# Optimization experiments

Hardware: AMD Instinct MI355X
Metric: run time of the kernel (lower is better)

Reference implementation:

```python
import jax, jax.numpy as jnp
import numpy as np

N = 100_000          # nodes
E = 1_600_000        # edges (avg degree 16)
IN_C, OUT_C = 256, 128


def setup_inputs() -> dict:
    key = jax.random.key(0)
    k1, k2, k3, k4, k5 = jax.random.split(key, 5)
    X = jax.random.normal(k1, (N, IN_C), dtype=jnp.float32)
    # nn.Linear(in, out, bias=False) weight has shape [out, in]
    W = jax.random.normal(k2, (OUT_C, IN_C), dtype=jnp.float32) * (1.0 / np.sqrt(IN_C))
    A_rows = jnp.sort(jax.random.randint(k3, (E,), 0, N, dtype=jnp.int32))
    A_cols = jax.random.randint(k4, (E,), 0, N, dtype=jnp.int32)
    # positive values mimicking symmetric-normalized adjacency entries
    A_vals = jax.random.uniform(k5, (E,), dtype=jnp.float32) * (1.0 / 16.0)
    return {"X": X, "W": W, "A_rows": A_rows, "A_cols": A_cols, "A_vals": A_vals}


def reference(X, W, A_rows, A_cols, A_vals):
    # X = self._linear(X)  ->  X @ W^T   [N, OUT_C]
    H = jnp.einsum("ni,oi->no", X, W)
    # X = torch.sparse.mm(A_hat, X): out[r] += v * H[c] for each edge (r, c, v)
    msgs = A_vals[:, None] * H[A_cols]                      # [E, OUT_C]
    out = jax.ops.segment_sum(msgs, A_rows, num_segments=N)  # [N, OUT_C]
    return out
```

## Files before the change

kernel.cpp:

```cpp
#include <hip/hip_runtime.h>
#include <hip/hip_bf16.h>

#define NNODES 100000
#define NEDGES 1600000
#define IN_C   256
#define OUT_C  128

typedef short bf16x8 __attribute__((ext_vector_type(8)));
typedef float f32x4  __attribute__((ext_vector_type(4)));

static __device__ __forceinline__ unsigned short f2bf(float f) {
    union { float f; unsigned u; } c; c.f = f;
    unsigned r = c.u + 0x7fffu + ((c.u >> 16) & 1u);
    return (unsigned short)(r >> 16);
}

union BF8 { bf16x8 v; unsigned short s[8]; };

__global__ __launch_bounds__(512, 4) void gemm_xwt(const float* __restrict__ X,
                                                   const float* __restrict__ W,
                                                   unsigned char* __restrict__ H8,
                                                   float* __restrict__ scale) {
    __shared__ unsigned short Wsh[128 * 256];

    const int tid  = threadIdx.x;
    const int lane = tid & 63;
    const int wid  = tid >> 6;

#pragma unroll
    for (int p = 0; p < 16; ++p) {
        int idx = p * 512 + tid;
        int n   = idx >> 6;
        int c4  = idx & 63;
        float4 v = *(const float4*)(W + (size_t)n * IN_C + c4 * 4);
        int byte = (n * 512 + c4 * 8) ^ ((n & 7) << 4);
        *(ushort4*)((char*)Wsh + byte) =
            make_ushort4(f2bf(v.x), f2bf(v.y), f2bf(v.z), f2bf(v.w));
    }
    __syncthreads();

    const int r0   = blockIdx.x * 128 + wid * 16;
    int arow = r0 + (lane & 15);
    if (arow > NNODES - 1) arow = NNODES - 1;
    const float* xrow = X + (size_t)arow * IN_C + (lane >> 4) * 8;

    f32x4 acc[8] = {};
#pragma unroll
    for (int ks = 0; ks < 8; ++ks) {
        float4 a0 = *(const float4*)(xrow + ks * 32);
        float4 a1 = *(const float4*)(xrow + ks * 32 + 4);
        BF8 t;
        t.s[0] = f2bf(a0.x); t.s[1] = f2bf(a0.y); t.s[2] = f2bf(a0.z); t.s[3] = f2bf(a0.w);
        t.s[4] = f2bf(a1.x); t.s[5] = f2bf(a1.y); t.s[6] = f2bf(a1.z); t.s[7] = f2bf(a1.w);
        const int kb = ks * 64 + (lane >> 4) * 16;
#pragma unroll
        for (int n8 = 0; n8 < 8; ++n8) {
            int nr   = n8 * 16 + (lane & 15);
            int byte = (nr * 512 + kb) ^ ((nr & 7) << 4);
            bf16x8 b = *(const bf16x8*)((const char*)Wsh + byte);
            acc[n8] = __builtin_amdgcn_mfma_f32_16x16x32_bf16(t.v, b, acc[n8],
                                                              0, 0, 0);
        }
    }

    float amax[4];
#pragma unroll
    for (int r = 0; r < 4; ++r) {
        float m = 0.f;
#pragma unroll
        for (int n8 = 0; n8 < 8; ++n8) m = fmaxf(m, fabsf(acc[n8][r]));
        amax[r] = m;
    }
#pragma unroll
    for (int d = 1; d < 16; d <<= 1)
#pragma unroll
        for (int r = 0; r < 4; ++r)
            amax[r] = fmaxf(amax[r], __shfl_xor(amax[r], d));

#pragma unroll
    for (int r = 0; r < 4; ++r) {
        int grow = r0 + (lane >> 4) * 4 + r;
        if (grow < NNODES) {
            float am  = amax[r];
            float inv = am > 0.f ? 127.f / am : 0.f;
            if ((lane & 15) == 0) scale[grow] = am * (1.f / 127.f);
#pragma unroll
            for (int n8 = 0; n8 < 8; ++n8) {
                float q = rintf(acc[n8][r] * inv);
                q = fminf(127.f, fmaxf(-127.f, q));
                H8[(size_t)grow * OUT_C + n8 * 16 + (lane & 15)] =
                    (unsigned char)((int)q + 128);
            }
        }
    }
}

__global__ __launch_bounds__(256) void build_rowptr(const int* __restrict__ rows,
                                                    int* __restrict__ rowptr) {
    int r = blockIdx.x * 256 + threadIdx.x;
    if (r > NNODES) return;
    int lo = 0, hi = NEDGES;
    while (lo < hi) {
        int mid = (lo + hi) >> 1;
        if (rows[mid] < r) lo = mid + 1; else hi = mid;
    }
    rowptr[r] = lo;
}

static __device__ __forceinline__ void fma8(float acc[8], float* sw,
                                            uint2 u, float v) {
    *sw += v;
    acc[0] += v * (float)( u.x        & 0xffu);
    acc[1] += v * (float)((u.x >>  8) & 0xffu);
    acc[2] += v * (float)((u.x >> 16) & 0xffu);
    acc[3] += v * (float)( u.x >> 24);
    acc[4] += v * (float)( u.y        & 0xffu);
    acc[5] += v * (float)((u.y >>  8) & 0xffu);
    acc[6] += v * (float)((u.y >> 16) & 0xffu);
    acc[7] += v * (float)( u.y >> 24);
}

__global__ __launch_bounds__(256) void spmm_rows(const uint2* __restrict__ H2,
                                                 const int* __restrict__ rowptr,
                                                 const int* __restrict__ cols,
                                                 const float* __restrict__ vals,
                                                 const float* __restrict__ scale,
                                                 float* __restrict__ out) {
    const int wid  = threadIdx.x >> 6;
    const int lane = threadIdx.x & 63;
    const int g    = lane >> 4;
    const int cg   = lane & 15;

    const int rowA = (blockIdx.x * 4 + wid) * 2;
    const int sA = rowptr[rowA];
    const int eA = rowptr[rowA + 1];
    const int eB = rowptr[rowA + 2];

    float accA[8], accB[8];
#pragma unroll
    for (int t = 0; t < 8; ++t) { accA[t] = 0.f; accB[t] = 0.f; }
    float swA = 0.f, swB = 0.f;

    int baseA = sA, baseB = eA;
    while (baseA < eA || baseB < eB) {
        int cntA = eA - baseA; cntA = cntA < 0 ? 0 : (cntA > 64 ? 64 : cntA);
        int cntB = eB - baseB; cntB = cntB < 0 ? 0 : (cntB > 64 ? 64 : cntB);

        int   ecA = 0, ecB = 0;
        float evA = 0.f, evB = 0.f;
        if (lane < cntA) { ecA = cols[baseA + lane]; evA = vals[baseA + lane] * scale[ecA]; }
        if (lane < cntB) { ecB = cols[baseB + lane]; evB = vals[baseB + lane] * scale[ecB]; }

        const int mx = cntA > cntB ? cntA : cntB;
        for (int j = 0; j < mx; j += 16) {
            const bool dA0 = j      < cntA, dA1 = j +  4 < cntA,
                       dA2 = j + 8  < cntA, dA3 = j + 12 < cntA;
            const bool dB0 = j      < cntB, dB1 = j +  4 < cntB,
                       dB2 = j + 8  < cntB, dB3 = j + 12 < cntB;

            int cA0 = __shfl(ecA, j + g),      cB0 = __shfl(ecB, j + g);
            int cA1 = __shfl(ecA, j + 4 + g),  cB1 = __shfl(ecB, j + 4 + g);
            int cA2 = __shfl(ecA, j + 8 + g),  cB2 = __shfl(ecB, j + 8 + g);
            int cA3 = __shfl(ecA, j + 12 + g), cB3 = __shfl(ecB, j + 12 + g);
            uint2 uA0, uA1, uA2, uA3, uB0, uB1, uB2, uB3;
            if (dA0) uA0 = H2[(size_t)cA0 * 16 + cg];
            if (dB0) uB0 = H2[(size_t)cB0 * 16 + cg];
            if (dA1) uA1 = H2[(size_t)cA1 * 16 + cg];
            if (dB1) uB1 = H2[(size_t)cB1 * 16 + cg];
            if (dA2) uA2 = H2[(size_t)cA2 * 16 + cg];
            if (dB2) uB2 = H2[(size_t)cB2 * 16 + cg];
            if (dA3) uA3 = H2[(size_t)cA3 * 16 + cg];
            if (dB3) uB3 = H2[(size_t)cB3 * 16 + cg];

            if (dA0) fma8(accA, &swA, uA0, __shfl(evA, j + g));
            if (dB0) fma8(accB, &swB, uB0, __shfl(evB, j + g));
            if (dA1) fma8(accA, &swA, uA1, __shfl(evA, j + 4 + g));
            if (dB1) fma8(accB, &swB, uB1, __shfl(evB, j + 4 + g));
            if (dA2) fma8(accA, &swA, uA2, __shfl(evA, j + 8 + g));
            if (dB2) fma8(accB, &swB, uB2, __shfl(evB, j + 8 + g));
            if (dA3) fma8(accA, &swA, uA3, __shfl(evA, j + 12 + g));
            if (dB3) fma8(accB, &swB, uB3, __shfl(evB, j + 12 + g));
        }

        baseA += cntA;
        baseB += cntB;
    }

#pragma unroll
    for (int t = 0; t < 8; ++t) {
        accA[t] += __shfl_xor(accA[t], 16);
        accA[t] += __shfl_xor(accA[t], 32);
        accB[t] += __shfl_xor(accB[t], 16);
        accB[t] += __shfl_xor(accB[t], 32);
    }
    swA += __shfl_xor(swA, 16); swA += __shfl_xor(swA, 32);
    swB += __shfl_xor(swB, 16); swB += __shfl_xor(swB, 32);

    if (lane < 16) {
        const float bA = 128.f * swA, bB = 128.f * swB;
        f32x4 a0 = { accA[0] - bA, accA[1] - bA, accA[2] - bA, accA[3] - bA };
        f32x4 a1 = { accA[4] - bA, accA[5] - bA, accA[6] - bA, accA[7] - bA };
        f32x4 b0 = { accB[0] - bB, accB[1] - bB, accB[2] - bB, accB[3] - bB };
        f32x4 b1 = { accB[4] - bB, accB[5] - bB, accB[6] - bB, accB[7] - bB };
        __builtin_nontemporal_store(a0, (f32x4*)(out + (size_t)rowA * OUT_C + cg * 8));
        __builtin_nontemporal_store(a1, (f32x4*)(out + (size_t)rowA * OUT_C + cg * 8 + 4));
        __builtin_nontemporal_store(b0, (f32x4*)(out + (size_t)(rowA + 1) * OUT_C + cg * 8));
        __builtin_nontemporal_store(b1, (f32x4*)(out + (size_t)(rowA + 1) * OUT_C + cg * 8 + 4));
    }
}

extern "C" void kernel_launch(void* const* d_in, const int* in_sizes, int n_in,
                              void* d_out, int out_size, void* d_ws, size_t ws_size,
                              hipStream_t stream) {
    const float* X      = (const float*)d_in[0];
    const float* W      = (const float*)d_in[1];
    const int*   A_rows = (const int*)d_in[2];
    const int*   A_cols = (const int*)d_in[3];
    const float* A_vals = (const float*)d_in[4];
    float* out = (float*)d_out;

    unsigned char* H8    = (unsigned char*)d_ws;
    float*         scale = (float*)((char*)d_ws + (size_t)NNODES * OUT_C);
    int*           rowptr = (int*)((char*)scale + (size_t)NNODES * sizeof(float));

    gemm_xwt<<<(NNODES + 127) / 128, 512, 0, stream>>>(X, W, H8, scale);
    build_rowptr<<<(NNODES + 1 + 255) / 256, 256, 0, stream>>>(A_rows, rowptr);
    spmm_rows<<<(NNODES + 7) / 8, 256, 0, stream>>>((const uint2*)H8, rowptr,
                                                    A_cols, A_vals, scale, out);
}
```

Before: 94.86 us.

## Process four rows per wave in SpMM and prefetch X in GEMM

The SpMM kernel now has each wavefront handle four CSR rows at once instead of two. Gathers from the int8 H table are interleaved across the rows in groups of eight edges per step, so more independent loads are in flight per wave. The GEMM kernel software-prefetches the next K-slice of X before converting and running the MFMAs on the current one. The cost is more registers per wave (four accumulator sets), which may lower occupancy, and more wasted work when row degrees are uneven.

```diff
diff --git a/kernel.cpp b/kernel.cpp
--- a/kernel.cpp
+++ b/kernel.cpp
@@ -45,10 +45,15 @@
     const float* xrow = X + (size_t)arow * IN_C + (lane >> 4) * 8;
 
     f32x4 acc[8] = {};
+    float4 a0 = *(const float4*)(xrow);
+    float4 a1 = *(const float4*)(xrow + 4);
 #pragma unroll
     for (int ks = 0; ks < 8; ++ks) {
-        float4 a0 = *(const float4*)(xrow + ks * 32);
-        float4 a1 = *(const float4*)(xrow + ks * 32 + 4);
+        float4 n0, n1;
+        if (ks < 7) {
+            n0 = *(const float4*)(xrow + (ks + 1) * 32);
+            n1 = *(const float4*)(xrow + (ks + 1) * 32 + 4);
+        }
         BF8 t;
         t.s[0] = f2bf(a0.x); t.s[1] = f2bf(a0.y); t.s[2] = f2bf(a0.z); t.s[3] = f2bf(a0.w);
         t.s[4] = f2bf(a1.x); t.s[5] = f2bf(a1.y); t.s[6] = f2bf(a1.z); t.s[7] = f2bf(a1.w);
@@ -61,6 +66,7 @@
             acc[n8] = __builtin_amdgcn_mfma_f32_16x16x32_bf16(t.v, b, acc[n8],
                                                               0, 0, 0);
         }
+        if (ks < 7) { a0 = n0; a1 = n1; }
     }
 
     float amax[4];
@@ -107,8 +113,13 @@
     rowptr[r] = lo;
 }
 
-static __device__ __forceinline__ void fma8(float acc[8], float* sw,
-                                            uint2 u, float v) {
+static __device__ __forceinline__ void edge4u(float acc[8], float* sw,
+                                              int ec, float ev, int jg,
+                                              const uint2* __restrict__ H2,
+                                              int cg) {
+    int   c = __shfl(ec, jg);
+    float v = __shfl(ev, jg);
+    uint2 u = H2[(size_t)c * 16 + cg];
     *sw += v;
     acc[0] += v * (float)( u.x        & 0xffu);
     acc[1] += v * (float)((u.x >>  8) & 0xffu);
@@ -131,81 +142,82 @@
     const int g    = lane >> 4;
     const int cg   = lane & 15;
 
-    const int rowA = (blockIdx.x * 4 + wid) * 2;
-    const int sA = rowptr[rowA];
-    const int eA = rowptr[rowA + 1];
-    const int eB = rowptr[rowA + 2];
-
-    float accA[8], accB[8];
-#pragma unroll
-    for (int t = 0; t < 8; ++t) { accA[t] = 0.f; accB[t] = 0.f; }
-    float swA = 0.f, swB = 0.f;
-
-    int baseA = sA, baseB = eA;
-    while (baseA < eA || baseB < eB) {
-        int cntA = eA - baseA; cntA = cntA < 0 ? 0 : (cntA > 64 ? 64 : cntA);
-        int cntB = eB - baseB; cntB = cntB < 0 ? 0 : (cntB > 64 ? 64 : cntB);
-
-        int   ecA = 0, ecB = 0;
-        float evA = 0.f, evB = 0.f;
+    const int rowA = (blockIdx.x * 4 + wid) * 4;
+    const int p0 = rowptr[rowA];
+    const int p1 = rowptr[rowA + 1];
+    const int p2 = rowptr[rowA + 2];
+    const int p3 = rowptr[rowA + 3];
+    const int p4 = rowptr[rowA + 4];
+
+    float accA[8], accB[8], accC[8], accD[8];
+#pragma unroll
+    for (int t = 0; t < 8; ++t) { accA[t] = 0.f; accB[t] = 0.f;
+                                  accC[t] = 0.f; accD[t] = 0.f; }
+    float swA = 0.f, swB = 0.f, swC = 0.f, swD = 0.f;
+
+    int baseA = p0, baseB = p1, baseC = p2, baseD = p3;
+    while (baseA < p1 || baseB < p2 || baseC < p3 || baseD < p4) {
+        int cntA = p1 - baseA; cntA = cntA < 0 ? 0 : (cntA > 64 ? 64 : cntA);
+        int cntB = p2 - baseB; cntB = cntB < 0 ? 0 : (cntB > 64 ? 64 : cntB);
+        int cntC = p3 - baseC; cntC = cntC < 0 ? 0 : (cntC > 64 ? 64 : cntC);
+        int cntD = p4 - baseD; cntD = cntD < 0 ? 0 : (cntD > 64 ? 64 : cntD);
+
+        int   ecA = 0, ecB = 0, ecC = 0, ecD = 0;
+        float evA = 0.f, evB = 0.f, evC = 0.f, evD = 0.f;
         if (lane < cntA) { ecA = cols[baseA + lane]; evA = vals[baseA + lane] * scale[ecA]; }
         if (lane < cntB) { ecB = cols[baseB + lane]; evB = vals[baseB + lane] * scale[ecB]; }
-
-        const int mx = cntA > cntB ? cntA : cntB;
-        for (int j = 0; j < mx; j += 16) {
-            const bool dA0 = j      < cntA, dA1 = j +  4 < cntA,
-                       dA2 = j + 8  < cntA, dA3 = j + 12 < cntA;
-            const bool dB0 = j      < cntB, dB1 = j +  4 < cntB,
-                       dB2 = j + 8  < cntB, dB3 = j + 12 < cntB;
-
-            int cA0 = __shfl(ecA, j + g),      cB0 = __shfl(ecB, j + g);
-            int cA1 = __shfl(ecA, j + 4 + g),  cB1 = __shfl(ecB, j + 4 + g);
-            int cA2 = __shfl(ecA, j + 8 + g),  cB2 = __shfl(ecB, j + 8 + g);
-            int cA3 = __shfl(ecA, j + 12 + g), cB3 = __shfl(ecB, j + 12 + g);
-            uint2 uA0, uA1, uA2, uA3, uB0, uB1, uB2, uB3;
-            if (dA0) uA0 = H2[(size_t)cA0 * 16 + cg];
-            if (dB0) uB0 = H2[(size_t)cB0 * 16 + cg];
-            if (dA1) uA1 = H2[(size_t)cA1 * 16 + cg];
-            if (dB1) uB1 = H2[(size_t)cB1 * 16 + cg];
-            if (dA2) uA2 = H2[(size_t)cA2 * 16 + cg];
-            if (dB2) uB2 = H2[(size_t)cB2 * 16 + cg];
-            if (dA3) uA3 = H2[(size_t)cA3 * 16 + cg];
-            if (dB3) uB3 = H2[(size_t)cB3 * 16 + cg];
-
-            if (dA0) fma8(accA, &swA, uA0, __shfl(evA, j + g));
-            if (dB0) fma8(accB, &swB, uB0, __shfl(evB, j + g));
-            if (dA1) fma8(accA, &swA, uA1, __shfl(evA, j + 4 + g));
-            if (dB1) fma8(accB, &swB, uB1, __shfl(evB, j + 4 + g));
-            if (dA2) fma8(accA, &swA, uA2, __shfl(evA, j + 8 + g));
-            if (dB2) fma8(accB, &swB, uB2, __shfl(evB, j + 8 + g));
-            if (dA3) fma8(accA, &swA, uA3, __shfl(evA, j + 12 + g));
-            if (dB3) fma8(accB, &swB, uB3, __shfl(evB, j + 12 + g));
-        }
-
-        baseA += cntA;
-        baseB += cntB;
+        if (lane < cntC) { ecC = cols[baseC + lane]; evC = vals[baseC + lane] * scale[ecC]; }
+        if (lane < cntD) { ecD = cols[baseD + lane]; evD = vals[baseD + lane] * scale[ecD]; }
+
+        int mx = cntA > cntB ? cntA : cntB;
+        mx = mx > cntC ? mx : cntC;
+        mx = mx > cntD ? mx : cntD;
+        for (int j = 0; j < mx; j += 8) {
+            if (j < cntA)     edge4u(accA, &swA, ecA, evA, j + g,     H2, cg);
+            if (j < cntB)     edge4u(accB, &swB, ecB, evB, j + g,     H2, cg);
+            if (j < cntC)     edge4u(accC, &swC, ecC, evC, j + g,     H2, cg);
+            if (j < cntD)     edge4u(accD, &swD, ecD, evD, j + g,     H2, cg);
+            if (j + 4 < cntA) edge4u(accA, &swA, ecA, evA, j + 4 + g, H2, cg);
+            if (j + 4 < cntB) edge4u(accB, &swB, ecB, evB, j + 4 + g, H2, cg);
+            if (j + 4 < cntC) edge4u(accC, &swC, ecC, evC, j + 4 + g, H2, cg);
+            if (j + 4 < cntD) edge4u(accD, &swD, ecD, evD, j + 4 + g, H2, cg);
+        }
+
+        baseA += cntA; baseB += cntB; baseC += cntC; baseD += cntD;
     }
 
 #pragma unroll
     for (int t = 0; t < 8; ++t) {
-        accA[t] += __shfl_xor(accA[t], 16);
-        accA[t] += __shfl_xor(accA[t], 32);
-        accB[t] += __shfl_xor(accB[t], 16);
-        accB[t] += __shfl_xor(accB[t], 32);
+        accA[t] += __shfl_xor(accA[t], 16); accA[t] += __shfl_xor(accA[t], 32);
+        accB[t] += __shfl_xor(accB[t], 16); accB[t] += __shfl_xor(accB[t], 32);
+        accC[t] += __shfl_xor(accC[t], 16); accC[t] += __shfl_xor(accC[t], 32);
+        accD[t] += __shfl_xor(accD[t], 16); accD[t] += __shfl_xor(accD[t], 32);
     }
     swA += __shfl_xor(swA, 16); swA += __shfl_xor(swA, 32);
     swB += __shfl_xor(swB, 16); swB += __shfl_xor(swB, 32);
+    swC += __shfl_xor(swC, 16); swC += __shfl_xor(swC, 32);
+    swD += __shfl_xor(swD, 16); swD += __shfl_xor(swD, 32);
 
     if (lane < 16) {
         const float bA = 128.f * swA, bB = 128.f * swB;
+        const float bC = 128.f * swC, bD = 128.f * swD;
         f32x4 a0 = { accA[0] - bA, accA[1] - bA, accA[2] - bA, accA[3] - bA };
         f32x4 a1 = { accA[4] - bA, accA[5] - bA, accA[6] - bA, accA[7] - bA };
         f32x4 b0 = { accB[0] - bB, accB[1] - bB, accB[2] - bB, accB[3] - bB };
         f32x4 b1 = { accB[4] - bB, accB[5] - bB, accB[6] - bB, accB[7] - bB };
-        __builtin_nontemporal_store(a0, (f32x4*)(out + (size_t)rowA * OUT_C + cg * 8));
-        __builtin_nontemporal_store(a1, (f32x4*)(out + (size_t)rowA * OUT_C + cg * 8 + 4));
-        __builtin_nontemporal_store(b0, (f32x4*)(out + (size_t)(rowA + 1) * OUT_C + cg * 8));
-        __builtin_nontemporal_store(b1, (f32x4*)(out + (size_t)(rowA + 1) * OUT_C + cg * 8 + 4));
+        f32x4 c0 = { accC[0] - bC, accC[1] - bC, accC[2] - bC, accC[3] - bC };
+        f32x4 c1 = { accC[4] - bC, accC[5] - bC, accC[6] - bC, accC[7] - bC };
+        f32x4 d0 = { accD[0] - bD, accD[1] - bD, accD[2] - bD, accD[3] - bD };
+        f32x4 d1 = { accD[4] - bD, accD[5] - bD, accD[6] - bD, accD[7] - bD };
+        float* o = out + (size_t)rowA * OUT_C + cg * 8;
+        __builtin_nontemporal_store(a0, (f32x4*)(o));
+        __builtin_nontemporal_store(a1, (f32x4*)(o + 4));
+        __builtin_nontemporal_store(b0, (f32x4*)(o + OUT_C));
+        __builtin_nontemporal_store(b1, (f32x4*)(o + OUT_C + 4));
+        __builtin_nontemporal_store(c0, (f32x4*)(o + 2 * OUT_C));
+        __builtin_nontemporal_store(c1, (f32x4*)(o + 2 * OUT_C + 4));
+        __builtin_nontemporal_store(d0, (f32x4*)(o + 3 * OUT_C));
+        __builtin_nontemporal_store(d1, (f32x4*)(o + 3 * OUT_C + 4));
     }
 }
 
@@ -225,6 +237,6 @@
 
     gemm_xwt<<<(NNODES + 127) / 128, 512, 0, stream>>>(X, W, H8, scale);
     build_rowptr<<<(NNODES + 1 + 255) / 256, 256, 0, stream>>>(A_rows, rowptr);
-    spmm_rows<<<(NNODES + 7) / 8, 256, 0, stream>>>((const uint2*)H8, rowptr,
-                                                    A_cols, A_vals, scale, out);
-}
+    spmm_rows<<<(NNODES + 15) / 16, 256, 0, stream>>>((const uint2*)H8, rowptr,
+                                                      A_cols, A_vals, scale, out);
+}
```

Measured after the change: 104.1 us. 9.8% more time.

## Precompute scaled edge weights in prep kernel and simplify SpMM edge loop

Applied to the files above, without the earlier changes.

Edge weights are now multiplied by the per-source dequant scale once, in a merged prep kernel that also builds the row pointers. The SpMM inner loop drops the 64-edge chunking with shuffles and instead has each 16-lane group load its own column and weight directly, processing 8 edges per row per iteration. This removes the dependent scale gather and the shuffles from the SpMM critical path. In exchange it adds an extra pass over the edges with a 6.4MB write, and the SpMM loop now issues fewer loads in flight per iteration (4 instead of 8).

```diff
diff --git a/kernel.cpp b/kernel.cpp
--- a/kernel.cpp
+++ b/kernel.cpp
@@ -95,16 +95,29 @@
     }
 }
 
-__global__ __launch_bounds__(256) void build_rowptr(const int* __restrict__ rows,
-                                                    int* __restrict__ rowptr) {
-    int r = blockIdx.x * 256 + threadIdx.x;
-    if (r > NNODES) return;
-    int lo = 0, hi = NEDGES;
-    while (lo < hi) {
-        int mid = (lo + hi) >> 1;
-        if (rows[mid] < r) lo = mid + 1; else hi = mid;
-    }
-    rowptr[r] = lo;
+#define RP_BLOCKS 392
+#define EV_BLOCKS ((NEDGES + 255) / 256)
+
+__global__ __launch_bounds__(256) void prep(const int* __restrict__ rows,
+                                            const int* __restrict__ cols,
+                                            const float* __restrict__ vals,
+                                            const float* __restrict__ scale,
+                                            int* __restrict__ rowptr,
+                                            float* __restrict__ ev) {
+    if (blockIdx.x < RP_BLOCKS) {
+        int r = blockIdx.x * 256 + threadIdx.x;
+        if (r > NNODES) return;
+        int lo = 0, hi = NEDGES;
+        while (lo < hi) {
+            int mid = (lo + hi) >> 1;
+            if (rows[mid] < r) lo = mid + 1; else hi = mid;
+        }
+        rowptr[r] = lo;
+    } else {
+        int e = (blockIdx.x - RP_BLOCKS) * 256 + threadIdx.x;
+        if (e < NEDGES)
+            ev[e] = vals[e] * scale[cols[e]];
+    }
 }
 
 static __device__ __forceinline__ void fma8(float acc[8], float* sw,
@@ -123,8 +136,7 @@
 __global__ __launch_bounds__(256) void spmm_rows(const uint2* __restrict__ H2,
                                                  const int* __restrict__ rowptr,
                                                  const int* __restrict__ cols,
-                                                 const float* __restrict__ vals,
-                                                 const float* __restrict__ scale,
+                                                 const float* __restrict__ ev,
                                                  float* __restrict__ out) {
     const int wid  = threadIdx.x >> 6;
     const int lane = threadIdx.x & 63;
@@ -141,49 +153,28 @@
     for (int t = 0; t < 8; ++t) { accA[t] = 0.f; accB[t] = 0.f; }
     float swA = 0.f, swB = 0.f;
 
-    int baseA = sA, baseB = eA;
-    while (baseA < eA || baseB < eB) {
-        int cntA = eA - baseA; cntA = cntA < 0 ? 0 : (cntA > 64 ? 64 : cntA);
-        int cntB = eB - baseB; cntB = cntB < 0 ? 0 : (cntB > 64 ? 64 : cntB);
-
-        int   ecA = 0, ecB = 0;
-        float evA = 0.f, evB = 0.f;
-        if (lane < cntA) { ecA = cols[baseA + lane]; evA = vals[baseA + lane] * scale[ecA]; }
-        if (lane < cntB) { ecB = cols[baseB + lane]; evB = vals[baseB + lane] * scale[ecB]; }
-
-        const int mx = cntA > cntB ? cntA : cntB;
-        for (int j = 0; j < mx; j += 16) {
-            const bool dA0 = j      < cntA, dA1 = j +  4 < cntA,
-                       dA2 = j + 8  < cntA, dA3 = j + 12 < cntA;
-            const bool dB0 = j      < cntB, dB1 = j +  4 < cntB,
-                       dB2 = j + 8  < cntB, dB3 = j + 12 < cntB;
-
-            int cA0 = __shfl(ecA, j + g),      cB0 = __shfl(ecB, j + g);
-            int cA1 = __shfl(ecA, j + 4 + g),  cB1 = __shfl(ecB, j + 4 + g);
-            int cA2 = __shfl(ecA, j + 8 + g),  cB2 = __shfl(ecB, j + 8 + g);
-            int cA3 = __shfl(ecA, j + 12 + g), cB3 = __shfl(ecB, j + 12 + g);
-            uint2 uA0, uA1, uA2, uA3, uB0, uB1, uB2, uB3;
-            if (dA0) uA0 = H2[(size_t)cA0 * 16 + cg];
-            if (dB0) uB0 = H2[(size_t)cB0 * 16 + cg];
-            if (dA1) uA1 = H2[(size_t)cA1 * 16 + cg];
-            if (dB1) uB1 = H2[(size_t)cB1 * 16 + cg];
-            if (dA2) uA2 = H2[(size_t)cA2 * 16 + cg];
-            if (dB2) uB2 = H2[(size_t)cB2 * 16 + cg];
-            if (dA3) uA3 = H2[(size_t)cA3 * 16 + cg];
-            if (dB3) uB3 = H2[(size_t)cB3 * 16 + cg];
-
-            if (dA0) fma8(accA, &swA, uA0, __shfl(evA, j + g));
-            if (dB0) fma8(accB, &swB, uB0, __shfl(evB, j + g));
-            if (dA1) fma8(accA, &swA, uA1, __shfl(evA, j + 4 + g));
-            if (dB1) fma8(accB, &swB, uB1, __shfl(evB, j + 4 + g));
-            if (dA2) fma8(accA, &swA, uA2, __shfl(evA, j + 8 + g));
-            if (dB2) fma8(accB, &swB, uB2, __shfl(evB, j + 8 + g));
-            if (dA3) fma8(accA, &swA, uA3, __shfl(evA, j + 12 + g));
-            if (dB3) fma8(accB, &swB, uB3, __shfl(evB, j + 12 + g));
-        }
-
-        baseA += cntA;
-        baseB += cntB;
+    int kA = sA, kB = eA;
+    while (kA < eA || kB < eB) {
+        const bool dA0 = kA + g     < eA, dA1 = kA + 4 + g < eA;
+        const bool dB0 = kB + g     < eB, dB1 = kB + 4 + g < eB;
+
+        int   cA0, cA1, cB0, cB1;
+        float vA0, vA1, vB0, vB1;
+        uint2 uA0, uA1, uB0, uB1;
+        if (dA0) { cA0 = cols[kA + g];     vA0 = ev[kA + g]; }
+        if (dB0) { cB0 = cols[kB + g];     vB0 = ev[kB + g]; }
+        if (dA1) { cA1 = cols[kA + 4 + g]; vA1 = ev[kA + 4 + g]; }
+        if (dB1) { cB1 = cols[kB + 4 + g]; vB1 = ev[kB + 4 + g]; }
+        if (dA0) uA0 = H2[(size_t)cA0 * 16 + cg];
+        if (dB0) uB0 = H2[(size_t)cB0 * 16 + cg];
+        if (dA1) uA1 = H2[(size_t)cA1 * 16 + cg];
+        if (dB1) uB1 = H2[(size_t)cB1 * 16 + cg];
+        if (dA0) fma8(accA, &swA, uA0, vA0);
+        if (dB0) fma8(accB, &swB, uB0, vB0);
+        if (dA1) fma8(accA, &swA, uA1, vA1);
+        if (dB1) fma8(accB, &swB, uB1, vB1);
+
+        kA += 8; kB += 8;
     }
 
 #pragma unroll
@@ -219,12 +210,14 @@
     const float* A_vals = (const float*)d_in[4];
     float* out = (float*)d_out;
 
-    unsigned char* H8    = (unsigned char*)d_ws;
-    float*         scale = (float*)((char*)d_ws + (size_t)NNODES * OUT_C);
+    unsigned char* H8     = (unsigned char*)d_ws;
+    float*         scale  = (float*)((char*)d_ws + (size_t)NNODES * OUT_C);
     int*           rowptr = (int*)((char*)scale + (size_t)NNODES * sizeof(float));
+    float*         ev     = (float*)((char*)rowptr + (size_t)(NNODES + 2) * sizeof(int));
 
     gemm_xwt<<<(NNODES + 127) / 128, 512, 0, stream>>>(X, W, H8, scale);
-    build_rowptr<<<(NNODES + 1 + 255) / 256, 256, 0, stream>>>(A_rows, rowptr);
+    prep<<<RP_BLOCKS + EV_BLOCKS, 256, 0, stream>>>(A_rows, A_cols, A_vals,
+                                                    scale, rowptr, ev);
     spmm_rows<<<(NNODES + 7) / 8, 256, 0, stream>>>((const uint2*)H8, rowptr,
-                                                    A_cols, A_vals, scale, out);
-}
+                                                    A_cols, ev, out);
+}
```

Result: slower. 102.0 us (+7.5%).
